# Kernel tuning notes

Measured on AMD Instinct MI355X. Metric: run time of the kernel, lower is better.

## Reference

```python
import jax, jax.numpy as jnp
import numpy as np

B, S, T, K = 96, 4, 16, 36           # groups, fixed 4 slots, max tags per slot, num boxes
V_DIM, Q_DIM, H = 1024, 512, 512


def setup_inputs() -> dict:
    key = jax.random.key(0)
    k_v, k_q, k_m, k_w1, k_b1, k_w2, k_b2 = jax.random.split(key, 7)

    # deterministic ragged lengths in [1, T], cyclic -> sum is exact
    lengths = (np.arange(B * S) % T) + 1              # [B*S], sum = 24 * 136 = 3264
    N = int(lengths.sum())                            # total rows in v / q
    # binary tag-attention mask: first `len` positions set per slot
    tags_attention = (np.arange(T)[None, :] < lengths[:, None]).astype(np.int32)
    tags_attention = jnp.asarray(tags_attention.reshape(B, S, T))

    v = jax.random.normal(k_v, (N, K, V_DIM), dtype=jnp.float32)
    q = jax.random.normal(k_q, (N, Q_DIM), dtype=jnp.float32)

    # box mask: random 0/1 but guarantee at least one valid box per group
    box_mask = (jax.random.uniform(k_m, (B, K)) < 0.9).astype(jnp.float32)
    box_mask = box_mask.at[:, 0].set(1.0)

    # FCNet (weight-normed Linear + ReLU; dropout inactive at eval) and scoring Linear
    w1 = jax.random.normal(k_w1, (V_DIM + Q_DIM, H), dtype=jnp.float32) * 0.02
    b1 = jax.random.normal(k_b1, (H,), dtype=jnp.float32) * 0.02
    w2 = jax.random.normal(k_w2, (H,), dtype=jnp.float32) * 0.02
    b2 = jax.random.normal(k_b2, (), dtype=jnp.float32) * 0.02

    return {"v": v, "q": q, "box_mask": box_mask, "tags_attention": tags_attention,
            "w1": w1, "b1": b1, "w2": w2, "b2": b2}


def reference(v, q, box_mask, tags_attention, w1, b1, w2, b2):
    N, Kb, _ = v.shape
    # logits: concat(v, q repeated over boxes) -> ReLU FC -> scalar score per box
    vq = jnp.concatenate([v, jnp.broadcast_to(q[:, None, :], (N, Kb, q.shape[-1]))], axis=-1)
    joint = jax.nn.relu(jnp.einsum('nkd,dh->nkh', vq, w1) + b1)      # [N, K, H]
    logits = jnp.einsum('nkh,h->nk', joint, w2) + b2                 # [N, K]

    # pad_sequence: ragged rows -> [B, S, T, K] via vectorized gather
    Bg, Sg, Tg = tags_attention.shape
    lengths = tags_attention.sum(-1).reshape(-1)                     # [B*S]
    starts = jnp.cumsum(lengths) - lengths                           # exclusive cumsum
    idx = starts[:, None] + jnp.arange(Tg)                           # [B*S, T]
    valid = jnp.arange(Tg)[None, :] < lengths[:, None]               # [B*S, T]
    gathered = jnp.take(logits, jnp.clip(idx, 0, N - 1), axis=0)     # [B*S, T, K]
    padded = jnp.where(valid[..., None], gathered, 0.0).reshape(Bg, Sg, Tg, Kb)

    # masked_softmax (allennlp-style) over the box dim with box_mask [B,1,1,K]
    mask = box_mask[:, None, None, :]
    s = jax.nn.softmax(padded * mask, axis=-1) * mask
    w = s / (s.sum(axis=-1, keepdims=True) + 1e-13)
    return w
```

## Files before the change

kernel.cpp:

```cpp
#include <hip/hip_runtime.h>
#include <cstdint>
#include <cstddef>

#define BB 96
#define SS 4
#define TT 16
#define KK 36
#define VDIM 1024
#define QDIM 512
#define HH 512
#define W1R 1536
#define NROWS 3264
#define MM (NROWS * KK)

typedef __attribute__((ext_vector_type(8))) short short8;
typedef __attribute__((ext_vector_type(4))) float f32x4;
typedef __attribute__((ext_vector_type(4))) unsigned short ushort4v;

static __device__ __forceinline__ unsigned short f2bf(float f) {
    union { float f; unsigned u; } v; v.f = f;
    unsigned u = v.u;
    u += 0x7FFFu + ((u >> 16) & 1u);
    return (unsigned short)(u >> 16);
}

__device__ __forceinline__ void gload_lds16(const void* g, void* l) {
    __builtin_amdgcn_global_load_lds(
        (const __attribute__((address_space(1))) unsigned int*)g,
        (__attribute__((address_space(3))) unsigned int*)l, 16, 0, 0);
}

#define SB() __builtin_amdgcn_sched_barrier(0)

__global__ __launch_bounds__(256) void prep_w1T(const float* __restrict__ w1,
                                                unsigned short* __restrict__ w1T) {
    int k = blockIdx.x * 256 + threadIdx.x;
    int c = blockIdx.y;
    w1T[(size_t)c * W1R + k] = f2bf(w1[(size_t)k * HH + c]);
}

__global__ __launch_bounds__(512) void starts_kernel(const int* __restrict__ tags,
                                                     int* __restrict__ starts,
                                                     int* __restrict__ lengths) {
    __shared__ int sl[BB * SS];
    int tid = threadIdx.x;
    int len = 0;
    if (tid < BB * SS) {
#pragma unroll
        for (int i = 0; i < TT; ++i) len += tags[tid * TT + i];
        sl[tid] = len;
    }
    __syncthreads();
    for (int off = 1; off < BB * SS; off <<= 1) {
        int v = 0;
        if (tid < BB * SS && tid >= off) v = sl[tid - off];
        __syncthreads();
        if (tid < BB * SS) sl[tid] += v;
        __syncthreads();
    }
    if (tid < BB * SS) { starts[tid] = sl[tid] - len; lengths[tid] = len; }
}

__global__ __launch_bounds__(256, 3) void qproj_mfma(const float* __restrict__ q,
                                                     const unsigned short* __restrict__ w1T,
                                                     const float* __restrict__ b1,
                                                     float* __restrict__ qp) {
    __shared__ __align__(16) unsigned short At[2][64 * 64];
    __shared__ __align__(16) unsigned short Bt[2][128 * 64];

    int tid = threadIdx.x, lane = tid & 63, wid = tid >> 6;
    int wm = wid >> 1, wn = wid & 1;
    int bx = blockIdx.x;
    int nb = bx & 3, mb = bx >> 2;
    int n0q = mb * 64, cb = nb * 128;
    int lr = lane & 15, lg = lane >> 4;

    const float* a_base = q + (size_t)(n0q + wid * 16 + (lane >> 4)) * QDIM + (lane & 15) * 4;
    const unsigned short* b_base = w1T + (size_t)(cb + wid * 32 + (lane >> 3)) * W1R + 1024
                                 + (((lane & 7) ^ (lane >> 3)) * 8);

    f32x4 acc[2][4];
#pragma unroll
    for (int mt = 0; mt < 2; ++mt)
#pragma unroll
        for (int nt = 0; nt < 4; ++nt) acc[mt][nt] = (f32x4){0.f, 0.f, 0.f, 0.f};

#define QP_CVT_WRITE(DST, AR)                                                  \
    _Pragma("unroll") for (int p = 0; p < 4; ++p) {                            \
        int r = wid * 16 + (lane >> 4) + p * 4;                                \
        int boff = r * 128 + ((((lane & 15) * 8)) ^ ((r & 7) << 4));           \
        unsigned short t4[4] = {f2bf(AR[p].x), f2bf(AR[p].y),                  \
                                f2bf(AR[p].z), f2bf(AR[p].w)};                 \
        *(ushort4v*)((char*)(DST) + boff) = *(const ushort4v*)t4;              \
    }

#define QP_COMPUTE(AC, BC)                                                     \
    _Pragma("unroll") for (int kk = 0; kk < 2; ++kk) {                         \
        short8 af[2], bf[4];                                                   \
        _Pragma("unroll") for (int mt = 0; mt < 2; ++mt) {                     \
            int R = wm * 32 + mt * 16 + lr;                                    \
            int off = R * 128 + ((kk * 64 + lg * 16) ^ ((R & 7) << 4));        \
            af[mt] = *(const short8*)((const char*)(AC) + off);                \
        }                                                                      \
        _Pragma("unroll") for (int nt = 0; nt < 4; ++nt) {                     \
            int R = wn * 64 + nt * 16 + lr;                                    \
            int off = R * 128 + ((kk * 64 + lg * 16) ^ ((R & 7) << 4));        \
            bf[nt] = *(const short8*)((const char*)(BC) + off);                \
        }                                                                      \
        __builtin_amdgcn_s_setprio(1);                                         \
        _Pragma("unroll") for (int mt = 0; mt < 2; ++mt)                       \
            _Pragma("unroll") for (int nt = 0; nt < 4; ++nt)                   \
                acc[mt][nt] = __builtin_amdgcn_mfma_f32_16x16x32_bf16(         \
                    af[mt], bf[nt], acc[mt][nt], 0, 0, 0);                     \
        __builtin_amdgcn_s_setprio(0);                                         \
    }

    {
        float4 ar[4];
#pragma unroll
        for (int p = 0; p < 4; ++p) ar[p] = *(const float4*)(a_base + (size_t)p * 4 * QDIM);
#pragma unroll
        for (int o = 0; o < 4; ++o)
            gload_lds16(b_base + (size_t)o * 8 * W1R, &Bt[0][(wid * 32 + o * 8) * 64]);
        SB();
        QP_CVT_WRITE(&At[0][0], ar)
    }
#pragma unroll 1
    for (int t = 0; t < 7; ++t) {
        int k0 = (t + 1) * 64;
        const unsigned short* Ac = &At[t & 1][0];
        const unsigned short* Bc = &Bt[t & 1][0];
        unsigned short* An = &At[(t + 1) & 1][0];
        unsigned short* Bn = &Bt[(t + 1) & 1][0];
        float4 ar[4];
#pragma unroll
        for (int p = 0; p < 4; ++p)
            ar[p] = *(const float4*)(a_base + (size_t)p * 4 * QDIM + k0);
#pragma unroll
        for (int o = 0; o < 4; ++o)
            gload_lds16(b_base + (size_t)o * 8 * W1R + k0, &Bn[(wid * 32 + o * 8) * 64]);
        SB();
        asm volatile("s_waitcnt vmcnt(8)" ::: "memory");
        asm volatile("s_waitcnt lgkmcnt(0)" ::: "memory");
        __builtin_amdgcn_s_barrier();
        SB();
        QP_COMPUTE(Ac, Bc)
        SB();
        QP_CVT_WRITE(An, ar)
    }
    SB();
    asm volatile("s_waitcnt vmcnt(0)" ::: "memory");
    asm volatile("s_waitcnt lgkmcnt(0)" ::: "memory");
    __builtin_amdgcn_s_barrier();
    SB();
    QP_COMPUTE(&At[1][0], &Bt[1][0])
#undef QP_COMPUTE
#undef QP_CVT_WRITE

#pragma unroll
    for (int nt = 0; nt < 4; ++nt) {
        int c = cb + wn * 64 + nt * 16 + lr;
        float b1v = b1[c];
#pragma unroll
        for (int mt = 0; mt < 2; ++mt)
#pragma unroll
            for (int r = 0; r < 4; ++r) {
                int row = wm * 32 + mt * 16 + lg * 4 + r;
                qp[(size_t)(n0q + row) * HH + c] = acc[mt][nt][r] + b1v;
            }
    }
}

__global__ __launch_bounds__(256, 3) void main_gemm(const float* __restrict__ v,
                                                    const unsigned short* __restrict__ w1T,
                                                    const float* __restrict__ qp,
                                                    const float* __restrict__ w2,
                                                    float* __restrict__ logits4) {
    __shared__ __align__(16) unsigned short At[128 * 64];
    __shared__ __align__(16) unsigned short Bt[2][128 * 64];

    int tid = threadIdx.x, lane = tid & 63, wid = tid >> 6;
    int wm = wid >> 1, wn = wid & 1;
    int bx = blockIdx.x;
    int orig = (bx & 7) * 459 + (bx >> 3);
    int nb = orig & 3, mb = orig >> 2;
    int m0 = mb * 128, cb = nb * 128;
    int lr = lane & 15, lg = lane >> 4;

    const float* a_base = v + (size_t)(m0 + wid * 32 + (lane >> 4)) * VDIM + (lane & 15) * 4;
    const unsigned short* b_base = w1T + (size_t)(cb + wid * 32 + (lane >> 3)) * W1R
                                 + (((lane & 7) ^ (lane >> 3)) * 8);

    f32x4 acc[4][4];
#pragma unroll
    for (int mt = 0; mt < 4; ++mt)
#pragma unroll
        for (int nt = 0; nt < 4; ++nt) acc[mt][nt] = (f32x4){0.f, 0.f, 0.f, 0.f};

#define MG_CVT_WRITE(DST, AR)                                                  \
    _Pragma("unroll") for (int p = 0; p < 8; ++p) {                            \
        int r = wid * 32 + (lane >> 4) + p * 4;                                \
        int boff = r * 128 + ((((lane & 15) * 8)) ^ ((r & 7) << 4));           \
        unsigned short t4[4] = {f2bf(AR[p].x), f2bf(AR[p].y),                  \
                                f2bf(AR[p].z), f2bf(AR[p].w)};                 \
        *(ushort4v*)((char*)(DST) + boff) = *(const ushort4v*)t4;              \
    }

#define MG_READ_AF()                                                           \
    _Pragma("unroll") for (int kk = 0; kk < 2; ++kk)                           \
        _Pragma("unroll") for (int mt = 0; mt < 4; ++mt) {                     \
            int R = wm * 64 + mt * 16 + lr;                                    \
            int off = R * 128 + ((kk * 64 + lg * 16) ^ ((R & 7) << 4));        \
            af[kk][mt] = *(const short8*)((const char*)&At[0] + off);          \
        }

#define MG_COMPUTE(BC)                                                         \
    _Pragma("unroll") for (int kk = 0; kk < 2; ++kk) {                         \
        short8 bf[4];                                                          \
        _Pragma("unroll") for (int nt = 0; nt < 4; ++nt) {                     \
            int R = wn * 64 + nt * 16 + lr;                                    \
            int off = R * 128 + ((kk * 64 + lg * 16) ^ ((R & 7) << 4));        \
            bf[nt] = *(const short8*)((const char*)(BC) + off);                \
        }                                                                      \
        __builtin_amdgcn_s_setprio(1);                                         \
        _Pragma("unroll") for (int mt = 0; mt < 4; ++mt)                       \
            _Pragma("unroll") for (int nt = 0; nt < 4; ++nt)                   \
                acc[mt][nt] = __builtin_amdgcn_mfma_f32_16x16x32_bf16(         \
                    af[kk][mt], bf[nt], acc[mt][nt], 0, 0, 0);                 \
        __builtin_amdgcn_s_setprio(0);                                         \
    }

    {
        float4 ar[8];
#pragma unroll
        for (int p = 0; p < 8; ++p) ar[p] = *(const float4*)(a_base + (size_t)p * 4 * VDIM);
#pragma unroll
        for (int o = 0; o < 4; ++o)
            gload_lds16(b_base + (size_t)o * 8 * W1R, &Bt[0][(wid * 32 + o * 8) * 64]);
        SB();
        MG_CVT_WRITE(&At[0], ar)
    }

#pragma unroll 1
    for (int t = 0; t < 15; ++t) {
        int k0 = (t + 1) * 64;
        const unsigned short* Bc = &Bt[t & 1][0];
        unsigned short* Bn = &Bt[(t + 1) & 1][0];
        float4 ar[8];
#pragma unroll
        for (int p = 0; p < 8; ++p)
            ar[p] = *(const float4*)(a_base + (size_t)p * 4 * VDIM + k0);
#pragma unroll
        for (int o = 0; o < 4; ++o)
            gload_lds16(b_base + (size_t)o * 8 * W1R + k0, &Bn[(wid * 32 + o * 8) * 64]);
        SB();
        asm volatile("s_waitcnt vmcnt(12)" ::: "memory");
        asm volatile("s_waitcnt lgkmcnt(0)" ::: "memory");
        __builtin_amdgcn_s_barrier();
        SB();
        short8 af[2][4];
        MG_READ_AF()
        SB();
        asm volatile("s_waitcnt lgkmcnt(0)" ::: "memory");
        __builtin_amdgcn_s_barrier();
        SB();
        MG_COMPUTE(Bc)
        SB();
        MG_CVT_WRITE(&At[0], ar)
    }
    SB();
    asm volatile("s_waitcnt vmcnt(0)" ::: "memory");
    asm volatile("s_waitcnt lgkmcnt(0)" ::: "memory");
    __builtin_amdgcn_s_barrier();
    SB();
    {
        short8 af[2][4];
        MG_READ_AF()
        MG_COMPUTE(&Bt[1][0])
    }
#undef MG_COMPUTE
#undef MG_READ_AF
#undef MG_CVT_WRITE

    __syncthreads();
    float* qs = (float*)&At[0];
    float* fl = qs + 5 * 128;
    int n0 = m0 / KK;
    for (int i = tid; i < 5 * 128; i += 256) {
        int nn = n0 + (i >> 7);
        if (nn >= NROWS) nn = NROWS - 1;
        qs[i] = qp[(size_t)nn * HH + cb + (i & 127)];
    }
    __syncthreads();

    float part[4][4] = {{0.f}};
#pragma unroll
    for (int nt = 0; nt < 4; ++nt) {
        int c = wn * 64 + nt * 16 + lr;
        float w2v = w2[cb + c];
#pragma unroll
        for (int mt = 0; mt < 4; ++mt)
#pragma unroll
            for (int r = 0; r < 4; ++r) {
                int row = wm * 64 + mt * 16 + lg * 4 + r;
                int ni = (m0 + row) / KK - n0;
                float pre = acc[mt][nt][r] + qs[ni * 128 + c];
                part[mt][r] += fmaxf(pre, 0.f) * w2v;
            }
    }
#pragma unroll
    for (int mt = 0; mt < 4; ++mt)
#pragma unroll
        for (int r = 0; r < 4; ++r) {
            float s = part[mt][r];
            s += __shfl_xor(s, 1, 64);
            s += __shfl_xor(s, 2, 64);
            s += __shfl_xor(s, 4, 64);
            s += __shfl_xor(s, 8, 64);
            if (lr == 0) fl[wn * 128 + wm * 64 + mt * 16 + lg * 4 + r] = s;
        }
    __syncthreads();
    if (tid < 128)
        logits4[(size_t)nb * MM + m0 + tid] = fl[tid] + fl[128 + tid];
}

__global__ __launch_bounds__(256) void softmax_kernel(const float* __restrict__ logits4,
                                                      const float* __restrict__ box_mask,
                                                      const int* __restrict__ starts,
                                                      const int* __restrict__ lengths,
                                                      float* __restrict__ out) {
    int lane = threadIdx.x & 63;
    int g = blockIdx.x * 4 + (threadIdx.x >> 6);
    int t   = g & (TT - 1);
    int row = g >> 4;
    int b   = row >> 2;

    int length = lengths[row];
    int start  = starts[row];

    int k = lane;
    bool kv = k < KK;
    float mval = kv ? box_mask[b * KK + k] : 0.f;
    bool act = kv && (mval != 0.f);

    float l = 0.f;
    if (act && t < length) {
        size_t idx = (size_t)(start + t) * KK + k;
        l = logits4[idx] + logits4[MM + idx] + logits4[2 * (size_t)MM + idx]
          + logits4[3 * (size_t)MM + idx];
    }

    float lm = act ? l : -1e30f;
#pragma unroll
    for (int off = 32; off >= 1; off >>= 1) lm = fmaxf(lm, __shfl_xor(lm, off, 64));

    float e = act ? expf(l - lm) : 0.f;
    float se = e;
#pragma unroll
    for (int off = 32; off >= 1; off >>= 1) se += __shfl_xor(se, off, 64);

    if (kv) out[(size_t)g * KK + k] = e / se;
}

extern "C" void kernel_launch(void* const* d_in, const int* in_sizes, int n_in,
                              void* d_out, int out_size, void* d_ws, size_t ws_size,
                              hipStream_t stream) {
    const float* v        = (const float*)d_in[0];
    const float* q        = (const float*)d_in[1];
    const float* box_mask = (const float*)d_in[2];
    const int*   tags     = (const int*)d_in[3];
    const float* w1       = (const float*)d_in[4];
    const float* b1       = (const float*)d_in[5];
    const float* w2       = (const float*)d_in[6];

    char* ws = (char*)d_ws;
    unsigned short* w1T   = (unsigned short*)ws;
    float* qp      = (float*)(ws + 1572864);
    float* logits4 = (float*)(ws + 1572864 + 6684672);
    int*   starts  = (int*)(ws + 1572864 + 6684672 + 1880064);
    int*   lengths = (int*)(ws + 1572864 + 6684672 + 1880064 + 1536);
    float* out     = (float*)d_out;

    hipLaunchKernelGGL(prep_w1T, dim3(6, 512), dim3(256), 0, stream, w1, w1T);
    hipLaunchKernelGGL(starts_kernel, dim3(1), dim3(512), 0, stream, tags, starts, lengths);
    hipLaunchKernelGGL(qproj_mfma, dim3((NROWS / 64) * 4), dim3(256), 0, stream,
                       q, w1T, b1, qp);
    hipLaunchKernelGGL(main_gemm, dim3((MM / 128) * 4), dim3(256), 0, stream,
                       v, w1T, qp, w2, logits4);
    hipLaunchKernelGGL(softmax_kernel, dim3((BB * SS * TT) / 4), dim3(256), 0, stream,
                       logits4, box_mask, starts, lengths, out);
}
```

Before: 237.3 us.

## Enlarge main GEMM tile to 256 rows with 8 waves and split-k interleaving

The main GEMM block now covers 256 M-rows instead of 128 and runs 512 threads. Each W1 tile in LDS is therefore reused by twice as many rows, and per-block B traffic is halved. The k-loop is restructured to issue the next B tile after the barrier and to alternate LDS fragment reads with MFMA over two half-k steps, which folds the epilogue iteration into the loop. The XCD block remap is adjusted for the new grid size. The risks are that __launch_bounds__(512,4) may force a very low VGPR budget and cause spills, and that the 64KB of LDS per block limits occupancy.

```diff
diff --git a/kernel.cpp b/kernel.cpp
--- a/kernel.cpp
+++ b/kernel.cpp
@@ -171,24 +171,26 @@
     }
 }
 
-__global__ __launch_bounds__(256, 3) void main_gemm(const float* __restrict__ v,
+__global__ __launch_bounds__(512, 4) void main_gemm(const float* __restrict__ v,
                                                     const unsigned short* __restrict__ w1T,
                                                     const float* __restrict__ qp,
                                                     const float* __restrict__ w2,
                                                     float* __restrict__ logits4) {
-    __shared__ __align__(16) unsigned short At[128 * 64];
+    __shared__ __align__(16) unsigned short At[256 * 64];
     __shared__ __align__(16) unsigned short Bt[2][128 * 64];
 
     int tid = threadIdx.x, lane = tid & 63, wid = tid >> 6;
     int wm = wid >> 1, wn = wid & 1;
     int bx = blockIdx.x;
-    int orig = (bx & 7) * 459 + (bx >> 3);
+    int xcd = bx & 7;
+    int base = (xcd < 4) ? xcd * 230 : 920 + (xcd - 4) * 229;
+    int orig = base + (bx >> 3);
     int nb = orig & 3, mb = orig >> 2;
-    int m0 = mb * 128, cb = nb * 128;
+    int m0 = mb * 256, cb = nb * 128;
     int lr = lane & 15, lg = lane >> 4;
 
     const float* a_base = v + (size_t)(m0 + wid * 32 + (lane >> 4)) * VDIM + (lane & 15) * 4;
-    const unsigned short* b_base = w1T + (size_t)(cb + wid * 32 + (lane >> 3)) * W1R
+    const unsigned short* b_base = w1T + (size_t)(cb + wid * 16 + (lane >> 3)) * W1R
                                  + (((lane & 7) ^ (lane >> 3)) * 8);
 
     f32x4 acc[4][4];
@@ -197,96 +199,92 @@
 #pragma unroll
         for (int nt = 0; nt < 4; ++nt) acc[mt][nt] = (f32x4){0.f, 0.f, 0.f, 0.f};
 
-#define MG_CVT_WRITE(DST, AR)                                                  \
+#define MG_CVT_WRITE(AR)                                                       \
     _Pragma("unroll") for (int p = 0; p < 8; ++p) {                            \
         int r = wid * 32 + (lane >> 4) + p * 4;                                \
         int boff = r * 128 + ((((lane & 15) * 8)) ^ ((r & 7) << 4));           \
         unsigned short t4[4] = {f2bf(AR[p].x), f2bf(AR[p].y),                  \
                                 f2bf(AR[p].z), f2bf(AR[p].w)};                 \
-        *(ushort4v*)((char*)(DST) + boff) = *(const ushort4v*)t4;              \
-    }
-
-#define MG_READ_AF()                                                           \
-    _Pragma("unroll") for (int kk = 0; kk < 2; ++kk)                           \
-        _Pragma("unroll") for (int mt = 0; mt < 4; ++mt) {                     \
-            int R = wm * 64 + mt * 16 + lr;                                    \
-            int off = R * 128 + ((kk * 64 + lg * 16) ^ ((R & 7) << 4));        \
-            af[kk][mt] = *(const short8*)((const char*)&At[0] + off);          \
-        }
-
-#define MG_COMPUTE(BC)                                                         \
-    _Pragma("unroll") for (int kk = 0; kk < 2; ++kk) {                         \
-        short8 bf[4];                                                          \
-        _Pragma("unroll") for (int nt = 0; nt < 4; ++nt) {                     \
-            int R = wn * 64 + nt * 16 + lr;                                    \
-            int off = R * 128 + ((kk * 64 + lg * 16) ^ ((R & 7) << 4));        \
-            bf[nt] = *(const short8*)((const char*)(BC) + off);                \
-        }                                                                      \
-        __builtin_amdgcn_s_setprio(1);                                         \
-        _Pragma("unroll") for (int mt = 0; mt < 4; ++mt)                       \
-            _Pragma("unroll") for (int nt = 0; nt < 4; ++nt)                   \
-                acc[mt][nt] = __builtin_amdgcn_mfma_f32_16x16x32_bf16(         \
-                    af[kk][mt], bf[nt], acc[mt][nt], 0, 0, 0);                 \
-        __builtin_amdgcn_s_setprio(0);                                         \
-    }
+        *(ushort4v*)((char*)&At[0] + boff) = *(const ushort4v*)t4;             \
+    }
+
+#define MG_READ_A(AF, KKC)                                                     \
+    _Pragma("unroll") for (int mt = 0; mt < 4; ++mt) {                         \
+        int R = wm * 64 + mt * 16 + lr;                                        \
+        int off = R * 128 + (((KKC) * 64 + lg * 16) ^ ((R & 7) << 4));         \
+        AF[mt] = *(const short8*)((const char*)&At[0] + off);                  \
+    }
+
+#define MG_READ_B(BF, BC, KKC)                                                 \
+    _Pragma("unroll") for (int nt = 0; nt < 4; ++nt) {                         \
+        int R = wn * 64 + nt * 16 + lr;                                        \
+        int off = R * 128 + (((KKC) * 64 + lg * 16) ^ ((R & 7) << 4));         \
+        BF[nt] = *(const short8*)((const char*)(BC) + off);                    \
+    }
+
+#define MG_MFMA(AF, BF)                                                        \
+    __builtin_amdgcn_s_setprio(1);                                             \
+    _Pragma("unroll") for (int mt = 0; mt < 4; ++mt)                           \
+        _Pragma("unroll") for (int nt = 0; nt < 4; ++nt)                       \
+            acc[mt][nt] = __builtin_amdgcn_mfma_f32_16x16x32_bf16(             \
+                AF[mt], BF[nt], acc[mt][nt], 0, 0, 0);                         \
+    __builtin_amdgcn_s_setprio(0);
 
     {
+#pragma unroll
+        for (int o = 0; o < 2; ++o)
+            gload_lds16(b_base + (size_t)o * 8 * W1R, &Bt[0][(wid * 16 + o * 8) * 64]);
         float4 ar[8];
 #pragma unroll
         for (int p = 0; p < 8; ++p) ar[p] = *(const float4*)(a_base + (size_t)p * 4 * VDIM);
-#pragma unroll
-        for (int o = 0; o < 4; ++o)
-            gload_lds16(b_base + (size_t)o * 8 * W1R, &Bt[0][(wid * 32 + o * 8) * 64]);
-        SB();
-        MG_CVT_WRITE(&At[0], ar)
+        SB();
+        MG_CVT_WRITE(ar)
     }
 
 #pragma unroll 1
-    for (int t = 0; t < 15; ++t) {
-        int k0 = (t + 1) * 64;
+    for (int t = 0; t < 16; ++t) {
+        int kA = (t < 15) ? (t + 1) * 64 : 960;
         const unsigned short* Bc = &Bt[t & 1][0];
         unsigned short* Bn = &Bt[(t + 1) & 1][0];
         float4 ar[8];
 #pragma unroll
         for (int p = 0; p < 8; ++p)
-            ar[p] = *(const float4*)(a_base + (size_t)p * 4 * VDIM + k0);
-#pragma unroll
-        for (int o = 0; o < 4; ++o)
-            gload_lds16(b_base + (size_t)o * 8 * W1R + k0, &Bn[(wid * 32 + o * 8) * 64]);
-        SB();
-        asm volatile("s_waitcnt vmcnt(12)" ::: "memory");
+            ar[p] = *(const float4*)(a_base + (size_t)p * 4 * VDIM + kA);
+        SB();
+        asm volatile("s_waitcnt vmcnt(8)" ::: "memory");
         asm volatile("s_waitcnt lgkmcnt(0)" ::: "memory");
         __builtin_amdgcn_s_barrier();
         SB();
-        short8 af[2][4];
-        MG_READ_AF()
+#pragma unroll
+        for (int o = 0; o < 2; ++o)
+            gload_lds16(b_base + (size_t)o * 8 * W1R + kA, Bn + (wid * 16 + o * 8) * 64);
+        SB();
+        {
+            short8 af0[4], bf0[4];
+            MG_READ_A(af0, 0)
+            MG_READ_B(bf0, Bc, 0)
+            MG_MFMA(af0, bf0)
+        }
+        short8 af1[4], bf1[4];
+        MG_READ_A(af1, 1)
+        MG_READ_B(bf1, Bc, 1)
         SB();
         asm volatile("s_waitcnt lgkmcnt(0)" ::: "memory");
         __builtin_amdgcn_s_barrier();
         SB();
-        MG_COMPUTE(Bc)
-        SB();
-        MG_CVT_WRITE(&At[0], ar)
-    }
-    SB();
-    asm volatile("s_waitcnt vmcnt(0)" ::: "memory");
-    asm volatile("s_waitcnt lgkmcnt(0)" ::: "memory");
-    __builtin_amdgcn_s_barrier();
-    SB();
-    {
-        short8 af[2][4];
-        MG_READ_AF()
-        MG_COMPUTE(&Bt[1][0])
-    }
-#undef MG_COMPUTE
-#undef MG_READ_AF
+        MG_MFMA(af1, bf1)
+        if (t < 15) { MG_CVT_WRITE(ar) }
+    }
+#undef MG_MFMA
+#undef MG_READ_A
+#undef MG_READ_B
 #undef MG_CVT_WRITE
 
     __syncthreads();
     float* qs = (float*)&At[0];
-    float* fl = qs + 5 * 128;
+    float* fl = qs + 9 * 128;
     int n0 = m0 / KK;
-    for (int i = tid; i < 5 * 128; i += 256) {
+    for (int i = tid; i < 9 * 128; i += 512) {
         int nn = n0 + (i >> 7);
         if (nn >= NROWS) nn = NROWS - 1;
         qs[i] = qp[(size_t)nn * HH + cb + (i & 127)];
@@ -317,11 +315,11 @@
             s += __shfl_xor(s, 2, 64);
             s += __shfl_xor(s, 4, 64);
             s += __shfl_xor(s, 8, 64);
-            if (lr == 0) fl[wn * 128 + wm * 64 + mt * 16 + lg * 4 + r] = s;
+            if (lr == 0) fl[wn * 256 + wm * 64 + mt * 16 + lg * 4 + r] = s;
         }
     __syncthreads();
-    if (tid < 128)
-        logits4[(size_t)nb * MM + m0 + tid] = fl[tid] + fl[128 + tid];
+    if (tid < 256)
+        logits4[(size_t)nb * MM + m0 + tid] = fl[tid] + fl[256 + tid];
 }
 
 __global__ __launch_bounds__(256) void softmax_kernel(const float* __restrict__ logits4,
@@ -385,7 +383,7 @@
     hipLaunchKernelGGL(starts_kernel, dim3(1), dim3(512), 0, stream, tags, starts, lengths);
     hipLaunchKernelGGL(qproj_mfma, dim3((NROWS / 64) * 4), dim3(256), 0, stream,
                        q, w1T, b1, qp);
-    hipLaunchKernelGGL(main_gemm, dim3((MM / 128) * 4), dim3(256), 0, stream,
+    hipLaunchKernelGGL(main_gemm, dim3((MM / 256) * 4), dim3(512), 0, stream,
                        v, w1T, qp, w2, logits4);
     hipLaunchKernelGGL(softmax_kernel, dim3((BB * SS * TT) / 4), dim3(256), 0, stream,
                        logits4, box_mask, starts, lengths, out);
```

New measurement: 254.5 us. +7.2%, slower.
